# Kernel tuning notes

Measured on AMD Instinct MI355X. Metric: run time of the kernel, lower is better.

Reference implementation:

```python
import jax, jax.numpy as jnp
import numpy as np

NU, NV, NE, EMB = 100000, 50000, 500000, 128


def _ln(x, g, b, eps=1e-5):
    mu = x.mean(-1, keepdims=True)
    var = ((x - mu) ** 2).mean(-1, keepdims=True)
    return (x - mu) * jax.lax.rsqrt(var + eps) * g + b


def setup_inputs() -> dict:
    key = jax.random.key(0)
    ks = jax.random.split(key, 12)
    s = 1.0 / np.sqrt(EMB).astype(np.float32)
    f32 = jnp.float32
    d = {
        "variable_emb": jax.random.normal(ks[0], (NU, EMB), f32),
        "edge_emb": jax.random.normal(ks[1], (NE, EMB), f32),
        "constraint_emb": jax.random.normal(ks[2], (NV, EMB), f32),
        "e_u": jax.random.randint(ks[3], (NE,), 0, NU),
        "e_v": jax.random.randint(ks[4], (NE,), 0, NV),
        # linear weights stored [in, out]; y = x @ W + b
        "W_left": jax.random.normal(ks[5], (EMB, EMB), f32) * s,
        "b_left": jnp.zeros((EMB,), f32),
        "W_edge": jax.random.normal(ks[6], (EMB, EMB), f32) * s,
        "W_right": jax.random.normal(ks[7], (EMB, EMB), f32) * s,
        "W_join": jax.random.normal(ks[8], (EMB, EMB), f32) * s,
        "b_join": jnp.zeros((EMB,), f32),
        "W_merge": jax.random.normal(ks[9], (2 * EMB, EMB), f32) * (s / np.sqrt(2.0).astype(np.float32)),
        "b_merge": jnp.zeros((EMB,), f32),
        # layernorm affine params
        "g_var": jnp.ones((EMB,), f32), "b_var": jnp.zeros((EMB,), f32),
        "g_edge": jnp.ones((EMB,), f32), "b_edge": jnp.zeros((EMB,), f32),
        "g_con": jnp.ones((EMB,), f32), "b_con": jnp.zeros((EMB,), f32),
        "g_join_ln": jnp.ones((EMB,), f32), "b_join_ln": jnp.zeros((EMB,), f32),
        "g_joint": jnp.ones((EMB,), f32), "b_joint": jnp.zeros((EMB,), f32),
        "g_merge": jnp.ones((EMB,), f32), "b_merge_ln": jnp.zeros((EMB,), f32),
    }
    return d


def reference(variable_emb, edge_emb, constraint_emb, e_u, e_v,
              W_left, b_left, W_edge, W_right, W_join, b_join, W_merge, b_merge,
              g_var, b_var, g_edge, b_edge, g_con, b_con,
              g_join_ln, b_join_ln, g_joint, b_joint, g_merge, b_merge_ln):

    def mp(v, e, c, var2con):
        v_t = _ln(v, g_var, b_var) @ W_left + b_left          # transform_left (with bias)
        e_t = _ln(e, g_edge, b_edge) @ W_edge                 # transform_edge (no bias)
        c_t = _ln(c, g_con, b_con) @ W_right                  # transform_right (no bias)
        # sparse.mm(var2edge.t(), v_t) == gather rows of v_t at e_u (values are ones)
        j = v_t[e_u] + e_t + c_t[e_v]                         # [NE, EMB]
        # transform_join = relu -> LayerNorm -> Linear, then norm_joint
        j = _ln(jax.nn.relu(j), g_join_ln, b_join_ln) @ W_join + b_join
        j = _ln(j, g_joint, b_joint)
        if var2con:
            agg = jax.ops.segment_sum(j, e_v, num_segments=NV)  # sparse.mm(con2edge, j)
            h = c_t
        else:
            agg = jax.ops.segment_sum(j, e_u, num_segments=NU)  # sparse.mm(var2edge, j)
            h = v_t
        out = jnp.concatenate([h, agg], axis=-1) @ W_merge + b_merge
        out = _ln(jax.nn.relu(out), g_merge, b_merge_ln)
        return h + out

    new_con = mp(variable_emb, edge_emb, constraint_emb, True)
    new_var = mp(variable_emb, edge_emb, new_con, False)
    return (new_var, new_con)
```

## Files before the change

### kernel.cpp

```cpp
#include <hip/hip_runtime.h>
#include <hip/hip_bf16.h>

#define NU_ 100000
#define NV_ 50000
#define NE_ 500000
#define EMB 128

typedef unsigned short u16;
typedef unsigned int u32;
typedef __attribute__((ext_vector_type(8))) short short8x;
typedef __attribute__((ext_vector_type(4))) float f32x4;

__device__ __forceinline__ float bf2f(u16 u) {
    union { u32 i; float f; } c; c.i = ((u32)u) << 16; return c.f;
}
__device__ __forceinline__ u16 f2bf(float f) {
    union { float f; u32 i; } c; c.f = f;
    u32 r = c.i + 0x7fffu + ((c.i >> 16) & 1u);
    return (u16)(r >> 16);
}

__global__ void convert_weights_kernel(
    const float* __restrict__ Wl, const float* __restrict__ We,
    const float* __restrict__ Wr, const float* __restrict__ Wj,
    const float* __restrict__ Wm,
    u16* __restrict__ wtl, u16* __restrict__ wte, u16* __restrict__ wtr,
    u16* __restrict__ wtj, u16* __restrict__ wtm)
{
    int b = blockIdx.x;
    const float* src; u16* dst; int K;
    if (b == 0)      { src = Wl; dst = wtl; K = 128; }
    else if (b == 1) { src = We; dst = wte; K = 128; }
    else if (b == 2) { src = Wr; dst = wtr; K = 128; }
    else if (b == 3) { src = Wj; dst = wtj; K = 128; }
    else             { src = Wm; dst = wtm; K = 256; }
    int total = K * 128;
    for (int i = threadIdx.x; i < total; i += blockDim.x) {
        int n = i / K, k = i - n * K;
        dst[i] = f2bf(src[(size_t)k * 128 + n]);
    }
}

__global__ __launch_bounds__(256) void ln_linear_kernel(
    const float* __restrict__ X, int Nrows,
    const float* __restrict__ g, const float* __restrict__ b,
    const u16* __restrict__ Wt, const float* __restrict__ bias,
    u16* __restrict__ Y)
{
    __shared__ __align__(16) u16 Asm[64][136];
    const int lane = threadIdx.x & 63, wv = threadIdx.x >> 6;
    const int ch = lane & 15, sub = lane >> 4;
    const int m0 = blockIdx.x * 64;
    const int rbase = wv * 16;

    float gv[8], bv[8];
#pragma unroll
    for (int j = 0; j < 8; ++j) { gv[j] = g[ch * 8 + j]; bv[j] = b[ch * 8 + j]; }

    for (int it = 0; it < 4; ++it) {
        int rl = rbase + it * 4 + sub;
        int row = m0 + rl;
        int rowc = row < Nrows ? row : Nrows - 1;
        const float* xr = X + (size_t)rowc * EMB + ch * 8;
        float4 a0 = *(const float4*)xr;
        float4 a1 = *(const float4*)(xr + 4);
        float x[8] = {a0.x, a0.y, a0.z, a0.w, a1.x, a1.y, a1.z, a1.w};
        float s = 0.f, ss = 0.f;
#pragma unroll
        for (int j = 0; j < 8; ++j) { s += x[j]; ss += x[j] * x[j]; }
#pragma unroll
        for (int m = 1; m < 16; m <<= 1) { s += __shfl_xor(s, m, 64); ss += __shfl_xor(ss, m, 64); }
        float mu = s * (1.0f / EMB);
        float rstd = rsqrtf(ss * (1.0f / EMB) - mu * mu + 1e-5f);
        u16 o[8];
#pragma unroll
        for (int j = 0; j < 8; ++j) o[j] = f2bf((x[j] - mu) * rstd * gv[j] + bv[j]);
        uint4 pk;
        pk.x = (u32)o[0] | ((u32)o[1] << 16);
        pk.y = (u32)o[2] | ((u32)o[3] << 16);
        pk.z = (u32)o[4] | ((u32)o[5] << 16);
        pk.w = (u32)o[6] | ((u32)o[7] << 16);
        *(uint4*)&Asm[rl][ch * 8] = pk;
    }
    __syncthreads();

    short8x afr[4];
#pragma unroll
    for (int kt = 0; kt < 4; ++kt)
        afr[kt] = *(const short8x*)&Asm[rbase + ch][kt * 32 + sub * 8];

#pragma unroll
    for (int nt = 0; nt < 8; ++nt) {
        float bz = bias ? bias[nt * 16 + ch] : 0.f;
        f32x4 acc = {bz, bz, bz, bz};
#pragma unroll
        for (int kt = 0; kt < 4; ++kt) {
            short8x bfr = *(const short8x*)(Wt + (size_t)(nt * 16 + ch) * 128 + kt * 32 + sub * 8);
            acc = __builtin_amdgcn_mfma_f32_16x16x32_bf16(afr[kt], bfr, acc, 0, 0, 0);
        }
#pragma unroll
        for (int r = 0; r < 4; ++r) {
            int row = m0 + rbase + sub * 4 + r;
            if (row < Nrows) Y[(size_t)row * EMB + nt * 16 + ch] = f2bf(acc[r]);
        }
    }
}

__global__ __launch_bounds__(256) void join_scatter_kernel(
    const float* __restrict__ Xe,
    const u16* __restrict__ v_t, const u16* __restrict__ c_t,
    const int* __restrict__ e_u, const int* __restrict__ e_v,
    const int* __restrict__ seg,
    const float* __restrict__ g_e, const float* __restrict__ b_e,
    const u16* __restrict__ Wt_e,
    const float* __restrict__ g1, const float* __restrict__ b1,
    const u16* __restrict__ Wt_j, const float* __restrict__ bias_j,
    const float* __restrict__ g2, const float* __restrict__ b2,
    float* __restrict__ agg)
{
    __shared__ __align__(16) u16 Asm[64][136];
    __shared__ __align__(16) u16 Esm[64][136];
    const int lane = threadIdx.x & 63, wv = threadIdx.x >> 6;
    const int ch = lane & 15, sub = lane >> 4;
    const int m0 = blockIdx.x * 64;
    const int rbase = wv * 16;

    float gev[8], bev[8];
#pragma unroll
    for (int j = 0; j < 8; ++j) { gev[j] = g_e[ch * 8 + j]; bev[j] = b_e[ch * 8 + j]; }

    for (int it = 0; it < 4; ++it) {
        int rl = rbase + it * 4 + sub;
        int edge = m0 + rl;
        int ec = edge < NE_ ? edge : NE_ - 1;
        const float* xr = Xe + (size_t)ec * EMB + ch * 8;
        float4 a0 = *(const float4*)xr;
        float4 a1 = *(const float4*)(xr + 4);
        float x[8] = {a0.x, a0.y, a0.z, a0.w, a1.x, a1.y, a1.z, a1.w};
        float s = 0.f, ss = 0.f;
#pragma unroll
        for (int j = 0; j < 8; ++j) { s += x[j]; ss += x[j] * x[j]; }
#pragma unroll
        for (int m = 1; m < 16; m <<= 1) { s += __shfl_xor(s, m, 64); ss += __shfl_xor(ss, m, 64); }
        float mu = s * (1.0f / EMB);
        float rstd = rsqrtf(ss * (1.0f / EMB) - mu * mu + 1e-5f);
        u16 o[8];
#pragma unroll
        for (int j = 0; j < 8; ++j) o[j] = f2bf((x[j] - mu) * rstd * gev[j] + bev[j]);
        uint4 pk;
        pk.x = (u32)o[0] | ((u32)o[1] << 16);
        pk.y = (u32)o[2] | ((u32)o[3] << 16);
        pk.z = (u32)o[4] | ((u32)o[5] << 16);
        pk.w = (u32)o[6] | ((u32)o[7] << 16);
        *(uint4*)&Asm[rl][ch * 8] = pk;
    }
    __syncthreads();

    {
        short8x afr[4];
#pragma unroll
        for (int kt = 0; kt < 4; ++kt)
            afr[kt] = *(const short8x*)&Asm[rbase + ch][kt * 32 + sub * 8];
#pragma unroll
        for (int nt = 0; nt < 8; ++nt) {
            f32x4 acc = {0.f, 0.f, 0.f, 0.f};
#pragma unroll
            for (int kt = 0; kt < 4; ++kt) {
                short8x bfr = *(const short8x*)(Wt_e + (size_t)(nt * 16 + ch) * 128 + kt * 32 + sub * 8);
                acc = __builtin_amdgcn_mfma_f32_16x16x32_bf16(afr[kt], bfr, acc, 0, 0, 0);
            }
#pragma unroll
            for (int r = 0; r < 4; ++r)
                Esm[rbase + sub * 4 + r][nt * 16 + ch] = f2bf(acc[r]);
        }
    }
    __syncthreads();

    float g1v[8], b1v[8];
#pragma unroll
    for (int j = 0; j < 8; ++j) { g1v[j] = g1[ch * 8 + j]; b1v[j] = b1[ch * 8 + j]; }
    for (int it = 0; it < 4; ++it) {
        int rl = rbase + it * 4 + sub;
        int edge = m0 + rl;
        int ec = edge < NE_ ? edge : NE_ - 1;
        int u = e_u[ec], vv = e_v[ec];
        uint4 vq = *(const uint4*)(v_t + (size_t)u * EMB + ch * 8);
        uint4 cq = *(const uint4*)(c_t + (size_t)vv * EMB + ch * 8);
        uint4 eq = *(const uint4*)&Esm[rl][ch * 8];
        u32 vw[4] = {vq.x, vq.y, vq.z, vq.w};
        u32 cw[4] = {cq.x, cq.y, cq.z, cq.w};
        u32 ew[4] = {eq.x, eq.y, eq.z, eq.w};
        float x[8];
#pragma unroll
        for (int j = 0; j < 4; ++j) {
            float v0 = bf2f((u16)(vw[j] & 0xffff)) + bf2f((u16)(cw[j] & 0xffff)) + bf2f((u16)(ew[j] & 0xffff));
            float v1 = bf2f((u16)(vw[j] >> 16)) + bf2f((u16)(cw[j] >> 16)) + bf2f((u16)(ew[j] >> 16));
            x[2 * j] = fmaxf(v0, 0.f);
            x[2 * j + 1] = fmaxf(v1, 0.f);
        }
        float s = 0.f, ss = 0.f;
#pragma unroll
        for (int j = 0; j < 8; ++j) { s += x[j]; ss += x[j] * x[j]; }
#pragma unroll
        for (int m = 1; m < 16; m <<= 1) { s += __shfl_xor(s, m, 64); ss += __shfl_xor(ss, m, 64); }
        float mu = s * (1.0f / EMB);
        float rstd = rsqrtf(ss * (1.0f / EMB) - mu * mu + 1e-5f);
        u16 o[8];
#pragma unroll
        for (int j = 0; j < 8; ++j) o[j] = f2bf((x[j] - mu) * rstd * g1v[j] + b1v[j]);
        uint4 pk;
        pk.x = (u32)o[0] | ((u32)o[1] << 16);
        pk.y = (u32)o[2] | ((u32)o[3] << 16);
        pk.z = (u32)o[4] | ((u32)o[5] << 16);
        pk.w = (u32)o[6] | ((u32)o[7] << 16);
        *(uint4*)&Asm[rl][ch * 8] = pk;
    }
    __syncthreads();

    short8x afr[4];
#pragma unroll
    for (int kt = 0; kt < 4; ++kt)
        afr[kt] = *(const short8x*)&Asm[rbase + ch][kt * 32 + sub * 8];

    f32x4 jacc[8];
#pragma unroll
    for (int nt = 0; nt < 8; ++nt) {
        float bz = bias_j[nt * 16 + ch];
        f32x4 acc = {bz, bz, bz, bz};
#pragma unroll
        for (int kt = 0; kt < 4; ++kt) {
            short8x bfr = *(const short8x*)(Wt_j + (size_t)(nt * 16 + ch) * 128 + kt * 32 + sub * 8);
            acc = __builtin_amdgcn_mfma_f32_16x16x32_bf16(afr[kt], bfr, acc, 0, 0, 0);
        }
        jacc[nt] = acc;
    }

    float g2v[8], b2v[8];
#pragma unroll
    for (int nt = 0; nt < 8; ++nt) { g2v[nt] = g2[nt * 16 + ch]; b2v[nt] = b2[nt * 16 + ch]; }

#pragma unroll
    for (int r = 0; r < 4; ++r) {
        float s = 0.f, ss = 0.f;
#pragma unroll
        for (int nt = 0; nt < 8; ++nt) { float v = jacc[nt][r]; s += v; ss += v * v; }
#pragma unroll
        for (int m = 1; m < 16; m <<= 1) { s += __shfl_xor(s, m, 64); ss += __shfl_xor(ss, m, 64); }
        float mu = s * (1.0f / EMB);
        float rstd = rsqrtf(ss * (1.0f / EMB) - mu * mu + 1e-5f);
        int edge = m0 + rbase + sub * 4 + r;
        if (edge < NE_) {
            int sg = seg[edge];
            float* dst = agg + (size_t)sg * EMB + ch;
#pragma unroll
            for (int nt = 0; nt < 8; ++nt) {
                float val = (jacc[nt][r] - mu) * rstd * g2v[nt] + b2v[nt];
                atomicAdd(dst + nt * 16, val);
            }
        }
    }
}

__global__ __launch_bounds__(256) void merge_kernel(
    const u16* __restrict__ h, const float* __restrict__ agg, int Nrows,
    const u16* __restrict__ Wt_m,
    const float* __restrict__ bias, const float* __restrict__ g,
    const float* __restrict__ bln,
    float* __restrict__ out)
{
    __shared__ __align__(16) u16 Asm[64][264];
    const int lane = threadIdx.x & 63, wv = threadIdx.x >> 6;
    const int ch = lane & 15, sub = lane >> 4;
    const int m0 = blockIdx.x * 64;
    const int rbase = wv * 16;

    for (int it = 0; it < 4; ++it) {
        int rl = rbase + it * 4 + sub;
        int row = m0 + rl;
        int rowc = row < Nrows ? row : Nrows - 1;
        uint4 hq = *(const uint4*)(h + (size_t)rowc * EMB + ch * 8);
        *(uint4*)&Asm[rl][ch * 8] = hq;
        const float* ar = agg + (size_t)rowc * EMB + ch * 8;
        float4 a0 = *(const float4*)ar;
        float4 a1 = *(const float4*)(ar + 4);
        float x[8] = {a0.x, a0.y, a0.z, a0.w, a1.x, a1.y, a1.z, a1.w};
        u16 o[8];
#pragma unroll
        for (int j = 0; j < 8; ++j) o[j] = f2bf(x[j]);
        uint4 pk;
        pk.x = (u32)o[0] | ((u32)o[1] << 16);
        pk.y = (u32)o[2] | ((u32)o[3] << 16);
        pk.z = (u32)o[4] | ((u32)o[5] << 16);
        pk.w = (u32)o[6] | ((u32)o[7] << 16);
        *(uint4*)&Asm[rl][128 + ch * 8] = pk;
    }
    __syncthreads();

    short8x afr[8];
#pragma unroll
    for (int kt = 0; kt < 8; ++kt)
        afr[kt] = *(const short8x*)&Asm[rbase + ch][kt * 32 + sub * 8];

    f32x4 macc[8];
#pragma unroll
    for (int nt = 0; nt < 8; ++nt) {
        float bz = bias[nt * 16 + ch];
        f32x4 acc = {bz, bz, bz, bz};
#pragma unroll
        for (int kt = 0; kt < 8; ++kt) {
            short8x bfr = *(const short8x*)(Wt_m + (size_t)(nt * 16 + ch) * 256 + kt * 32 + sub * 8);
            acc = __builtin_amdgcn_mfma_f32_16x16x32_bf16(afr[kt], bfr, acc, 0, 0, 0);
        }
        macc[nt] = acc;
    }

    float gm[8], bm[8];
#pragma unroll
    for (int nt = 0; nt < 8; ++nt) { gm[nt] = g[nt * 16 + ch]; bm[nt] = bln[nt * 16 + ch]; }

#pragma unroll
    for (int r = 0; r < 4; ++r) {
        float s = 0.f, ss = 0.f;
#pragma unroll
        for (int nt = 0; nt < 8; ++nt) { float v = fmaxf(macc[nt][r], 0.f); s += v; ss += v * v; }
#pragma unroll
        for (int m = 1; m < 16; m <<= 1) { s += __shfl_xor(s, m, 64); ss += __shfl_xor(ss, m, 64); }
        float mu = s * (1.0f / EMB);
        float rstd = rsqrtf(ss * (1.0f / EMB) - mu * mu + 1e-5f);
        int row = m0 + rbase + sub * 4 + r;
        if (row < Nrows) {
#pragma unroll
            for (int nt = 0; nt < 8; ++nt) {
                float v = fmaxf(macc[nt][r], 0.f);
                float o = (v - mu) * rstd * gm[nt] + bm[nt];
                float hv = bf2f(Asm[rbase + sub * 4 + r][nt * 16 + ch]);
                out[(size_t)row * EMB + nt * 16 + ch] = o + hv;
            }
        }
    }
}

extern "C" void kernel_launch(void* const* d_in, const int* in_sizes, int n_in,
                              void* d_out, int out_size, void* d_ws, size_t ws_size,
                              hipStream_t stream) {
    const float* variable_emb   = (const float*)d_in[0];
    const float* edge_emb       = (const float*)d_in[1];
    const float* constraint_emb = (const float*)d_in[2];
    const int*   e_u            = (const int*)d_in[3];
    const int*   e_v            = (const int*)d_in[4];
    const float* W_left  = (const float*)d_in[5];
    const float* b_left  = (const float*)d_in[6];
    const float* W_edge  = (const float*)d_in[7];
    const float* W_right = (const float*)d_in[8];
    const float* W_join  = (const float*)d_in[9];
    const float* b_join  = (const float*)d_in[10];
    const float* W_merge = (const float*)d_in[11];
    const float* b_merge = (const float*)d_in[12];
    const float* g_var   = (const float*)d_in[13];
    const float* b_var   = (const float*)d_in[14];
    const float* g_edge  = (const float*)d_in[15];
    const float* b_edge  = (const float*)d_in[16];
    const float* g_con   = (const float*)d_in[17];
    const float* b_con   = (const float*)d_in[18];
    const float* g_join_ln = (const float*)d_in[19];
    const float* b_join_ln = (const float*)d_in[20];
    const float* g_joint   = (const float*)d_in[21];
    const float* b_joint   = (const float*)d_in[22];
    const float* g_merge   = (const float*)d_in[23];
    const float* b_merge_ln = (const float*)d_in[24];

    char* ws = (char*)d_ws;
    u16* wtl = (u16*)ws; ws += 128 * 128 * 2;
    u16* wte = (u16*)ws; ws += 128 * 128 * 2;
    u16* wtr = (u16*)ws; ws += 128 * 128 * 2;
    u16* wtj = (u16*)ws; ws += 128 * 128 * 2;
    u16* wtm = (u16*)ws; ws += 256 * 128 * 2;
    u16* v_t = (u16*)ws; ws += (size_t)NU_ * EMB * 2;
    u16* c_t = (u16*)ws; ws += (size_t)NV_ * EMB * 2;

    float* out_f   = (float*)d_out;
    float* new_var = out_f;
    float* new_con = out_f + (size_t)NU_ * EMB;
    float* agg = out_f;

    const int gb_v = (NU_ + 63) / 64;
    const int gb_c = (NV_ + 63) / 64;
    const int gb_e = (NE_ + 63) / 64;

    convert_weights_kernel<<<5, 256, 0, stream>>>(W_left, W_edge, W_right, W_join, W_merge,
                                                  wtl, wte, wtr, wtj, wtm);
    ln_linear_kernel<<<gb_v, 256, 0, stream>>>(variable_emb, NU_, g_var, b_var, wtl, b_left, v_t);
    ln_linear_kernel<<<gb_c, 256, 0, stream>>>(constraint_emb, NV_, g_con, b_con, wtr, nullptr, c_t);
    hipMemsetAsync(agg, 0, (size_t)NV_ * EMB * sizeof(float), stream);
    join_scatter_kernel<<<gb_e, 256, 0, stream>>>(edge_emb, v_t, c_t, e_u, e_v, e_v,
                                                  g_edge, b_edge, wte,
                                                  g_join_ln, b_join_ln, wtj, b_join,
                                                  g_joint, b_joint, agg);
    merge_kernel<<<gb_c, 256, 0, stream>>>(c_t, agg, NV_, wtm, b_merge, g_merge, b_merge_ln, new_con);

    ln_linear_kernel<<<gb_c, 256, 0, stream>>>(new_con, NV_, g_con, b_con, wtr, nullptr, c_t);
    hipMemsetAsync(agg, 0, (size_t)NU_ * EMB * sizeof(float), stream);
    join_scatter_kernel<<<gb_e, 256, 0, stream>>>(edge_emb, v_t, c_t, e_u, e_v, e_u,
                                                  g_edge, b_edge, wte,
                                                  g_join_ln, b_join_ln, wtj, b_join,
                                                  g_joint, b_joint, agg);
    merge_kernel<<<gb_v, 256, 0, stream>>>(v_t, agg, NU_, wtm, b_merge, g_merge, b_merge_ln, new_var);
}
```

Baseline: 1.372 ms.

## Precompute edge transform once and reuse it across both message passes

Adds an et_kernel that computes LayerNorm(edge_emb) @ W_edge once into a bf16 workspace buffer. A new join kernel then reads this buffer instead of recomputing the edge LayerNorm and GEMM in each of the two passes. This removes one full edge LN+GEMM and replaces the fp32 edge read (256 B/row) with a bf16 read (128 B/row) in each pass. In exchange it writes and reads an extra 128 MB buffer and needs enough workspace, with a fallback to the old path otherwise.

```diff
diff --git a/kernel.cpp b/kernel.cpp
--- a/kernel.cpp
+++ b/kernel.cpp
@@ -19,6 +19,7 @@
     u32 r = c.i + 0x7fffu + ((c.i >> 16) & 1u);
     return (u16)(r >> 16);
 }
+
 
 __global__ void convert_weights_kernel(
     const float* __restrict__ Wl, const float* __restrict__ We,
@@ -102,6 +103,179 @@
         for (int r = 0; r < 4; ++r) {
             int row = m0 + rbase + sub * 4 + r;
             if (row < Nrows) Y[(size_t)row * EMB + nt * 16 + ch] = f2bf(acc[r]);
+        }
+    }
+}
+
+__global__ __launch_bounds__(256) void et_kernel(
+    const float* __restrict__ Xe,
+    const float* __restrict__ g_e, const float* __restrict__ b_e,
+    const u16* __restrict__ Wt_e,
+    u16* __restrict__ e_t)
+{
+    __shared__ __align__(16) u16 Asm[64][136];
+    const int lane = threadIdx.x & 63, wv = threadIdx.x >> 6;
+    const int ch = lane & 15, sub = lane >> 4;
+    const int m0 = blockIdx.x * 64;
+    const int rbase = wv * 16;
+
+    float gev[8], bev[8];
+#pragma unroll
+    for (int j = 0; j < 8; ++j) { gev[j] = g_e[ch * 8 + j]; bev[j] = b_e[ch * 8 + j]; }
+
+    for (int it = 0; it < 4; ++it) {
+        int rl = rbase + it * 4 + sub;
+        int edge = m0 + rl;
+        int ec = edge < NE_ ? edge : NE_ - 1;
+        const float* xr = Xe + (size_t)ec * EMB + ch * 8;
+        float4 a0 = *(const float4*)xr;
+        float4 a1 = *(const float4*)(xr + 4);
+        float x[8] = {a0.x, a0.y, a0.z, a0.w, a1.x, a1.y, a1.z, a1.w};
+        float s = 0.f, ss = 0.f;
+#pragma unroll
+        for (int j = 0; j < 8; ++j) { s += x[j]; ss += x[j] * x[j]; }
+#pragma unroll
+        for (int m = 1; m < 16; m <<= 1) { s += __shfl_xor(s, m, 64); ss += __shfl_xor(ss, m, 64); }
+        float mu = s * (1.0f / EMB);
+        float rstd = rsqrtf(ss * (1.0f / EMB) - mu * mu + 1e-5f);
+        u16 o[8];
+#pragma unroll
+        for (int j = 0; j < 8; ++j) o[j] = f2bf((x[j] - mu) * rstd * gev[j] + bev[j]);
+        uint4 pk;
+        pk.x = (u32)o[0] | ((u32)o[1] << 16);
+        pk.y = (u32)o[2] | ((u32)o[3] << 16);
+        pk.z = (u32)o[4] | ((u32)o[5] << 16);
+        pk.w = (u32)o[6] | ((u32)o[7] << 16);
+        *(uint4*)&Asm[rl][ch * 8] = pk;
+    }
+    __syncthreads();
+
+    short8x afr[4];
+#pragma unroll
+    for (int kt = 0; kt < 4; ++kt)
+        afr[kt] = *(const short8x*)&Asm[rbase + ch][kt * 32 + sub * 8];
+#pragma unroll
+    for (int nt = 0; nt < 8; ++nt) {
+        f32x4 acc = {0.f, 0.f, 0.f, 0.f};
+#pragma unroll
+        for (int kt = 0; kt < 4; ++kt) {
+            short8x bfr = *(const short8x*)(Wt_e + (size_t)(nt * 16 + ch) * 128 + kt * 32 + sub * 8);
+            acc = __builtin_amdgcn_mfma_f32_16x16x32_bf16(afr[kt], bfr, acc, 0, 0, 0);
+        }
+#pragma unroll
+        for (int r = 0; r < 4; ++r) {
+            int edge = m0 + rbase + sub * 4 + r;
+            if (edge < NE_) e_t[(size_t)edge * EMB + nt * 16 + ch] = f2bf(acc[r]);
+        }
+    }
+}
+
+__global__ __launch_bounds__(256) void join_pre2_kernel(
+    const u16* __restrict__ e_t,
+    const u16* __restrict__ v_t, const u16* __restrict__ c_t,
+    const int* __restrict__ e_u, const int* __restrict__ e_v,
+    const int* __restrict__ seg,
+    const float* __restrict__ g1, const float* __restrict__ b1,
+    const u16* __restrict__ Wt_j, const float* __restrict__ bias_j,
+    const float* __restrict__ g2, const float* __restrict__ b2,
+    float* __restrict__ agg)
+{
+    __shared__ __align__(16) u16 Asm[64][136];
+    __shared__ __align__(16) u16 Esm[64][136];
+    const int lane = threadIdx.x & 63, wv = threadIdx.x >> 6;
+    const int ch = lane & 15, sub = lane >> 4;
+    const int m0 = blockIdx.x * 64;
+    const int rbase = wv * 16;
+
+    for (int it = 0; it < 4; ++it) {
+        int rl = rbase + it * 4 + sub;
+        int edge = m0 + rl;
+        int ec = edge < NE_ ? edge : NE_ - 1;
+        *(uint4*)&Esm[rl][ch * 8] = *(const uint4*)(e_t + (size_t)ec * EMB + ch * 8);
+    }
+    __syncthreads();
+
+    float g1v[8], b1v[8];
+#pragma unroll
+    for (int j = 0; j < 8; ++j) { g1v[j] = g1[ch * 8 + j]; b1v[j] = b1[ch * 8 + j]; }
+    for (int it = 0; it < 4; ++it) {
+        int rl = rbase + it * 4 + sub;
+        int edge = m0 + rl;
+        int ec = edge < NE_ ? edge : NE_ - 1;
+        int u = e_u[ec], vv = e_v[ec];
+        uint4 vq = *(const uint4*)(v_t + (size_t)u * EMB + ch * 8);
+        uint4 cq = *(const uint4*)(c_t + (size_t)vv * EMB + ch * 8);
+        uint4 eq = *(const uint4*)&Esm[rl][ch * 8];
+        u32 vw[4] = {vq.x, vq.y, vq.z, vq.w};
+        u32 cw[4] = {cq.x, cq.y, cq.z, cq.w};
+        u32 ew[4] = {eq.x, eq.y, eq.z, eq.w};
+        float x[8];
+#pragma unroll
+        for (int j = 0; j < 4; ++j) {
+            float v0 = bf2f((u16)(vw[j] & 0xffff)) + bf2f((u16)(cw[j] & 0xffff)) + bf2f((u16)(ew[j] & 0xffff));
+            float v1 = bf2f((u16)(vw[j] >> 16)) + bf2f((u16)(cw[j] >> 16)) + bf2f((u16)(ew[j] >> 16));
+            x[2 * j] = fmaxf(v0, 0.f);
+            x[2 * j + 1] = fmaxf(v1, 0.f);
+        }
+        float s = 0.f, ss = 0.f;
+#pragma unroll
+        for (int j = 0; j < 8; ++j) { s += x[j]; ss += x[j] * x[j]; }
+#pragma unroll
+        for (int m = 1; m < 16; m <<= 1) { s += __shfl_xor(s, m, 64); ss += __shfl_xor(ss, m, 64); }
+        float mu = s * (1.0f / EMB);
+        float rstd = rsqrtf(ss * (1.0f / EMB) - mu * mu + 1e-5f);
+        u16 o[8];
+#pragma unroll
+        for (int j = 0; j < 8; ++j) o[j] = f2bf((x[j] - mu) * rstd * g1v[j] + b1v[j]);
+        uint4 pk;
+        pk.x = (u32)o[0] | ((u32)o[1] << 16);
+        pk.y = (u32)o[2] | ((u32)o[3] << 16);
+        pk.z = (u32)o[4] | ((u32)o[5] << 16);
+        pk.w = (u32)o[6] | ((u32)o[7] << 16);
+        *(uint4*)&Asm[rl][ch * 8] = pk;
+    }
+    __syncthreads();
+
+    short8x afr[4];
+#pragma unroll
+    for (int kt = 0; kt < 4; ++kt)
+        afr[kt] = *(const short8x*)&Asm[rbase + ch][kt * 32 + sub * 8];
+
+    f32x4 jacc[8];
+#pragma unroll
+    for (int nt = 0; nt < 8; ++nt) {
+        float bz = bias_j[nt * 16 + ch];
+        f32x4 acc = {bz, bz, bz, bz};
+#pragma unroll
+        for (int kt = 0; kt < 4; ++kt) {
+            short8x bfr = *(const short8x*)(Wt_j + (size_t)(nt * 16 + ch) * 128 + kt * 32 + sub * 8);
+            acc = __builtin_amdgcn_mfma_f32_16x16x32_bf16(afr[kt], bfr, acc, 0, 0, 0);
+        }
+        jacc[nt] = acc;
+    }
+
+    float g2v[8], b2v[8];
+#pragma unroll
+    for (int nt = 0; nt < 8; ++nt) { g2v[nt] = g2[nt * 16 + ch]; b2v[nt] = b2[nt * 16 + ch]; }
+
+#pragma unroll
+    for (int r = 0; r < 4; ++r) {
+        float s = 0.f, ss = 0.f;
+#pragma unroll
+        for (int nt = 0; nt < 8; ++nt) { float v = jacc[nt][r]; s += v; ss += v * v; }
+#pragma unroll
+        for (int m = 1; m < 16; m <<= 1) { s += __shfl_xor(s, m, 64); ss += __shfl_xor(ss, m, 64); }
+        float mu = s * (1.0f / EMB);
+        float rstd = rsqrtf(ss * (1.0f / EMB) - mu * mu + 1e-5f);
+        int edge = m0 + rbase + sub * 4 + r;
+        if (edge < NE_) {
+            int sg = seg[edge];
+            float* dst = agg + (size_t)sg * EMB + ch;
+#pragma unroll
+            for (int nt = 0; nt < 8; ++nt) {
+                float val = (jacc[nt][r] - mu) * rstd * g2v[nt] + b2v[nt];
+                atomicAdd(dst + nt * 16, val);
+            }
         }
     }
 }
@@ -377,6 +551,9 @@
     u16* wtm = (u16*)ws; ws += 256 * 128 * 2;
     u16* v_t = (u16*)ws; ws += (size_t)NU_ * EMB * 2;
     u16* c_t = (u16*)ws; ws += (size_t)NV_ * EMB * 2;
+    u16* e_t = (u16*)ws; ws += (size_t)NE_ * EMB * 2;
+    size_t ws_needed = (size_t)(ws - (char*)d_ws);
+    const bool have_et = ws_size >= ws_needed;
 
     float* out_f   = (float*)d_out;
     float* new_var = out_f;
@@ -391,18 +568,36 @@
                                                   wtl, wte, wtr, wtj, wtm);
     ln_linear_kernel<<<gb_v, 256, 0, stream>>>(variable_emb, NU_, g_var, b_var, wtl, b_left, v_t);
     ln_linear_kernel<<<gb_c, 256, 0, stream>>>(constraint_emb, NV_, g_con, b_con, wtr, nullptr, c_t);
-    hipMemsetAsync(agg, 0, (size_t)NV_ * EMB * sizeof(float), stream);
-    join_scatter_kernel<<<gb_e, 256, 0, stream>>>(edge_emb, v_t, c_t, e_u, e_v, e_v,
-                                                  g_edge, b_edge, wte,
-                                                  g_join_ln, b_join_ln, wtj, b_join,
-                                                  g_joint, b_joint, agg);
-    merge_kernel<<<gb_c, 256, 0, stream>>>(c_t, agg, NV_, wtm, b_merge, g_merge, b_merge_ln, new_con);
-
-    ln_linear_kernel<<<gb_c, 256, 0, stream>>>(new_con, NV_, g_con, b_con, wtr, nullptr, c_t);
-    hipMemsetAsync(agg, 0, (size_t)NU_ * EMB * sizeof(float), stream);
-    join_scatter_kernel<<<gb_e, 256, 0, stream>>>(edge_emb, v_t, c_t, e_u, e_v, e_u,
-                                                  g_edge, b_edge, wte,
-                                                  g_join_ln, b_join_ln, wtj, b_join,
-                                                  g_joint, b_joint, agg);
-    merge_kernel<<<gb_v, 256, 0, stream>>>(v_t, agg, NU_, wtm, b_merge, g_merge, b_merge_ln, new_var);
-}
+
+    if (have_et) {
+        et_kernel<<<gb_e, 256, 0, stream>>>(edge_emb, g_edge, b_edge, wte, e_t);
+
+        hipMemsetAsync(agg, 0, (size_t)NV_ * EMB * sizeof(float), stream);
+        join_pre2_kernel<<<gb_e, 256, 0, stream>>>(e_t, v_t, c_t, e_u, e_v, e_v,
+                                                   g_join_ln, b_join_ln, wtj, b_join,
+                                                   g_joint, b_joint, agg);
+        merge_kernel<<<gb_c, 256, 0, stream>>>(c_t, agg, NV_, wtm, b_merge, g_merge, b_merge_ln, new_con);
+
+        ln_linear_kernel<<<gb_c, 256, 0, stream>>>(new_con, NV_, g_con, b_con, wtr, nullptr, c_t);
+        hipMemsetAsync(agg, 0, (size_t)NU_ * EMB * sizeof(float), stream);
+        join_pre2_kernel<<<gb_e, 256, 0, stream>>>(e_t, v_t, c_t, e_u, e_v, e_u,
+                                                   g_join_ln, b_join_ln, wtj, b_join,
+                                                   g_joint, b_joint, agg);
+        merge_kernel<<<gb_v, 256, 0, stream>>>(v_t, agg, NU_, wtm, b_merge, g_merge, b_merge_ln, new_var);
+    } else {
+        hipMemsetAsync(agg, 0, (size_t)NV_ * EMB * sizeof(float), stream);
+        join_scatter_kernel<<<gb_e, 256, 0, stream>>>(edge_emb, v_t, c_t, e_u, e_v, e_v,
+                                                      g_edge, b_edge, wte,
+                                                      g_join_ln, b_join_ln, wtj, b_join,
+                                                      g_joint, b_joint, agg);
+        merge_kernel<<<gb_c, 256, 0, stream>>>(c_t, agg, NV_, wtm, b_merge, g_merge, b_merge_ln, new_con);
+
+        ln_linear_kernel<<<gb_c, 256, 0, stream>>>(new_con, NV_, g_con, b_con, wtr, nullptr, c_t);
+        hipMemsetAsync(agg, 0, (size_t)NU_ * EMB * sizeof(float), stream);
+        join_scatter_kernel<<<gb_e, 256, 0, stream>>>(edge_emb, v_t, c_t, e_u, e_v, e_u,
+                                                      g_edge, b_edge, wte,
+                                                      g_join_ln, b_join_ln, wtj, b_join,
+                                                      g_joint, b_joint, agg);
+        merge_kernel<<<gb_v, 256, 0, stream>>>(v_t, agg, NU_, wtm, b_merge, g_merge, b_merge_ln, new_var);
+    }
+}
```

After: 1.202 ms. 12.3% less time.
